# Kernel tuning notes

Measured on AMD Instinct MI355X. Metric: run time of the kernel, lower is better.

## Reference

```python
import jax, jax.numpy as jnp
import numpy as np

CHEBY = 3  # max_degree / number of Chebyshev polynomial orders
IN_F, OUT_F = 64, 64
B, N = 32, 2048


def setup_inputs() -> dict:
    key = jax.random.key(0)
    k1, k2, k3, k4, k5 = jax.random.split(key, 5)
    stdv = 1.0 / np.sqrt(OUT_F)
    stdv2 = 1.0  # 1/sqrt(K.size(1)) = 1/sqrt(1)
    x = jax.random.normal(k1, (B, N, IN_F), dtype=jnp.float32)
    adj = jax.random.uniform(k2, (B, N, N), dtype=jnp.float32)
    weight = jax.random.uniform(k3, (IN_F, OUT_F), minval=-stdv, maxval=stdv, dtype=jnp.float32)
    K = jax.random.uniform(k4, (CHEBY, 1), minval=-stdv2, maxval=stdv2, dtype=jnp.float32)
    bias = jax.random.uniform(k5, (OUT_F,), minval=-stdv, maxval=stdv, dtype=jnp.float32)
    return {"x": x, "adj": adj, "weight": weight, "K": K, "bias": bias}


def chebyshev_stack(x, adj, max_degree):
    # T_0 = x, T_1 = A x, T_k = 2 A T_{k-1} - T_{k-2}; stack along new last axis
    Ts = [x]
    if max_degree > 1:
        Ts.append(jnp.einsum('bnm,bmf->bnf', adj, x))
    for _ in range(2, max_degree):
        Ts.append(2.0 * jnp.einsum('bnm,bmf->bnf', adj, Ts[-1]) - Ts[-2])
    return jnp.stack(Ts, axis=-1)  # [B, N, F, K]


def reference(x, adj, weight, K, bias):
    support = chebyshev_stack(x, adj, CHEBY)            # [B, N, F, K]
    combined = jnp.einsum('bnfk,ko->bnf', support, K)   # K-weighted sum -> [B, N, F]
    out = jnp.einsum('bnf,fo->bno', combined, weight) + bias
    return out
```

## Files before the change

### kernel.cpp

```cpp
#include <hip/hip_runtime.h>
#include <stdint.h>

#define NN 2048
#define FF 64
#define NB 32

typedef __attribute__((ext_vector_type(8))) short bf16x8;
typedef __attribute__((ext_vector_type(4))) float f32x4;

__device__ __forceinline__ uint16_t f2bf(float f) {
  uint32_t u = __builtin_bit_cast(uint32_t, f);
  return (uint16_t)((u + 0x7FFFu + ((u >> 16) & 1u)) >> 16);
}
__device__ __forceinline__ float bf2f(uint16_t h) {
  uint32_t u = ((uint32_t)h) << 16;
  return __builtin_bit_cast(float, u);
}

__global__ void k_prep(const float* __restrict__ W, uint16_t* __restrict__ Wt) {
  int t = threadIdx.x;
  for (int i = 0; i < 16; ++i) {
    int idx = t * 16 + i;
    int k = idx >> 6, f = idx & 63;
    Wt[f * 64 + k] = f2bf(W[idx]);
  }
}

__global__ __launch_bounds__(256) void k_xw(const float* __restrict__ x,
                                            const uint16_t* __restrict__ Wt,
                                            uint16_t* __restrict__ xw) {
  __shared__ short As[64 * 72];
  int bid = blockIdx.x;
  int b = bid >> 5;
  int n0 = (bid & 31) * 64;
  int t = threadIdx.x;
  const float* xb = x + ((size_t)b * NN + n0) * FF;
  for (int i = 0; i < 4; ++i) {
    int idx = t + i * 256;
    int r = idx >> 4, c = (idx & 15) * 4;
    float4 v = *(const float4*)(xb + r * FF + c);
    uint32_t p0 = f2bf(v.x) | ((uint32_t)f2bf(v.y) << 16);
    uint32_t p1 = f2bf(v.z) | ((uint32_t)f2bf(v.w) << 16);
    uint2 pv = {p0, p1};
    *(uint2*)&As[r * 72 + c] = pv;
  }
  __syncthreads();
  int lane = t & 63, wave = t >> 6;
  int l16 = lane & 15, quad = lane >> 4;
  f32x4 acc[4] = {};
  for (int ks = 0; ks < 2; ++ks) {
    bf16x8 a = *(const bf16x8*)&As[(wave * 16 + l16) * 72 + ks * 32 + quad * 8];
    for (int fi = 0; fi < 4; ++fi) {
      bf16x8 bq = *(const bf16x8*)(Wt + (fi * 16 + l16) * 64 + ks * 32 + quad * 8);
      acc[fi] = __builtin_amdgcn_mfma_f32_16x16x32_bf16(a, bq, acc[fi], 0, 0, 0);
    }
  }
  for (int fi = 0; fi < 4; ++fi)
    for (int r = 0; r < 4; ++r) {
      int n = n0 + wave * 16 + quad * 4 + r;
      int f = fi * 16 + l16;
      xw[((size_t)b * NN + n) * FF + f] = f2bf(acc[fi][r]);
    }
}

__global__ __launch_bounds__(256) void k_tr(const uint16_t* __restrict__ src,
                                            uint16_t* __restrict__ dst) {
  __shared__ uint16_t T[64 * 72];
  int bid = blockIdx.x;
  int b = bid >> 5;
  int n0 = (bid & 31) * 64;
  int t = threadIdx.x;
  for (int j = 0; j < 2; ++j) {
    int n = (t >> 3) + j * 32;
    int f8 = (t & 7) * 8;
    uint4 v = *(const uint4*)(src + ((size_t)b * NN + n0 + n) * FF + f8);
    *(uint4*)&T[n * 72 + f8] = v;
  }
  __syncthreads();
  for (int j = 0; j < 2; ++j) {
    int f = (t >> 3) + j * 32;
    int n8 = (t & 7) * 8;
    uint4 v;
    uint16_t* tp = (uint16_t*)&v;
    for (int i = 0; i < 8; ++i) tp[i] = T[(n8 + i) * 72 + f];
    *(uint4*)(dst + ((size_t)b * FF + f) * NN + n0 + n8) = v;
  }
}

template <int EPI>
__global__ __launch_bounds__(256) void k_gemm(const float* __restrict__ adj,
                                              const uint16_t* __restrict__ Bt,
                                              uint16_t* __restrict__ Yb,
                                              const uint16_t* __restrict__ xw,
                                              const uint16_t* __restrict__ y1,
                                              const float* __restrict__ Kc,
                                              const float* __restrict__ bias,
                                              float* __restrict__ out) {
  __shared__ short As[128 * 72];
  __shared__ short Bs[64 * 72];
  int bid = blockIdx.x;
  int b = bid & 31;
  int row0 = (bid >> 5) * 128;
  int t = threadIdx.x;
  const float* Ab = adj + (size_t)b * NN * NN + (size_t)row0 * NN;
  const uint16_t* Btb = Bt + (size_t)b * FF * NN;

  int ar = t >> 4, ac4 = (t & 15) * 4;
  int bfb = t >> 3, bc8 = (t & 7) * 8;

  float4 areg[8];
  uint4 breg[2];
  for (int i = 0; i < 8; ++i)
    areg[i] = *(const float4*)(Ab + (size_t)(ar + i * 16) * NN + ac4);
  for (int j = 0; j < 2; ++j)
    breg[j] = *(const uint4*)(Btb + (size_t)(bfb + j * 32) * NN + bc8);

  f32x4 acc[2][4] = {};
  int lane = t & 63, wave = t >> 6;
  int l16 = lane & 15, quad = lane >> 4;

  for (int k0 = 0; k0 < NN; k0 += 64) {
    __syncthreads();
    for (int i = 0; i < 8; ++i) {
      float4 v = areg[i];
      uint32_t p0 = f2bf(v.x) | ((uint32_t)f2bf(v.y) << 16);
      uint32_t p1 = f2bf(v.z) | ((uint32_t)f2bf(v.w) << 16);
      uint2 pv = {p0, p1};
      *(uint2*)&As[(ar + i * 16) * 72 + ac4] = pv;
    }
    for (int j = 0; j < 2; ++j)
      *(uint4*)&Bs[(bfb + j * 32) * 72 + bc8] = breg[j];
    __syncthreads();
    if (k0 + 64 < NN) {
      for (int i = 0; i < 8; ++i)
        areg[i] = *(const float4*)(Ab + (size_t)(ar + i * 16) * NN + (k0 + 64) + ac4);
      for (int j = 0; j < 2; ++j)
        breg[j] = *(const uint4*)(Btb + (size_t)(bfb + j * 32) * NN + (k0 + 64) + bc8);
    }
    for (int ks = 0; ks < 2; ++ks) {
      bf16x8 af[2];
      for (int mi = 0; mi < 2; ++mi)
        af[mi] = *(const bf16x8*)&As[(wave * 32 + mi * 16 + l16) * 72 + ks * 32 + quad * 8];
      for (int fi = 0; fi < 4; ++fi) {
        bf16x8 bq = *(const bf16x8*)&Bs[(fi * 16 + l16) * 72 + ks * 32 + quad * 8];
        acc[0][fi] = __builtin_amdgcn_mfma_f32_16x16x32_bf16(af[0], bq, acc[0][fi], 0, 0, 0);
        acc[1][fi] = __builtin_amdgcn_mfma_f32_16x16x32_bf16(af[1], bq, acc[1][fi], 0, 0, 0);
      }
    }
  }

  if (EPI == 0) {
    for (int mi = 0; mi < 2; ++mi)
      for (int fi = 0; fi < 4; ++fi)
        for (int r = 0; r < 4; ++r) {
          int n = row0 + wave * 32 + mi * 16 + quad * 4 + r;
          int f = fi * 16 + l16;
          Yb[((size_t)b * NN + n) * FF + f] = f2bf(acc[mi][fi][r]);
        }
  } else {
    float ka = Kc[0] - Kc[2], kb = Kc[1], kc = 2.0f * Kc[2];
    for (int mi = 0; mi < 2; ++mi)
      for (int fi = 0; fi < 4; ++fi) {
        int f = fi * 16 + l16;
        float bv = bias[f];
        for (int r = 0; r < 4; ++r) {
          int n = row0 + wave * 32 + mi * 16 + quad * 4 + r;
          size_t idx = ((size_t)b * NN + n) * FF + f;
          out[idx] = ka * bf2f(xw[idx]) + kb * bf2f(y1[idx]) + kc * acc[mi][fi][r] + bv;
        }
      }
  }
}

extern "C" void kernel_launch(void* const* d_in, const int* in_sizes, int n_in,
                              void* d_out, int out_size, void* d_ws, size_t ws_size,
                              hipStream_t stream) {
  const float* x    = (const float*)d_in[0];
  const float* adj  = (const float*)d_in[1];
  const float* W    = (const float*)d_in[2];
  const float* K    = (const float*)d_in[3];
  const float* bias = (const float*)d_in[4];
  float* out = (float*)d_out;

  uint8_t* ws = (uint8_t*)d_ws;
  const size_t SZ = (size_t)NB * NN * FF * sizeof(uint16_t);
  uint16_t* xw_n = (uint16_t*)(ws);
  uint16_t* xwT  = (uint16_t*)(ws + SZ);
  uint16_t* y1_n = (uint16_t*)(ws + 2 * SZ);
  uint16_t* y1T  = (uint16_t*)(ws + 3 * SZ);
  uint16_t* Wt   = (uint16_t*)(ws + 4 * SZ);

  k_prep<<<dim3(1), dim3(256), 0, stream>>>(W, Wt);
  k_xw<<<dim3(1024), dim3(256), 0, stream>>>(x, Wt, xw_n);
  k_tr<<<dim3(1024), dim3(256), 0, stream>>>(xw_n, xwT);
  k_gemm<0><<<dim3(512), dim3(256), 0, stream>>>(adj, xwT, y1_n, nullptr, nullptr,
                                                 nullptr, nullptr, nullptr);
  k_tr<<<dim3(1024), dim3(256), 0, stream>>>(y1_n, y1T);
  k_gemm<1><<<dim3(512), dim3(256), 0, stream>>>(adj, y1T, nullptr, xw_n, y1_n,
                                                 K, bias, out);
}
```

Measured before the change: 936.4 us.

## Retile adjacency GEMM to 16-row blocks and fuse transposes into producers

The GEMM kernels now use 16-row tiles with 4096 blocks, each wave owning 16 output features. The B operand is read straight from global memory rather than staged in LDS, and A is staged in 256-wide K chunks. The separate transpose kernels are removed: the xw kernel and the first GEMM epilogue each write both the row-major and the transposed copy through a small LDS tile. This aims to raise occupancy and cut launches and extra passes over memory for this bandwidth-bound fp32 adj read, at the cost of less B reuse per block and more global reads of the B operand.

```diff
diff --git a/kernel.cpp b/kernel.cpp
--- a/kernel.cpp
+++ b/kernel.cpp
@@ -26,149 +26,125 @@
   }
 }
 
-__global__ __launch_bounds__(256) void k_xw(const float* __restrict__ x,
-                                            const uint16_t* __restrict__ Wt,
-                                            uint16_t* __restrict__ xw) {
-  __shared__ short As[64 * 72];
+__global__ __launch_bounds__(256, 4) void k_xw(const float* __restrict__ x,
+                                               const uint16_t* __restrict__ Wt,
+                                               uint16_t* __restrict__ xw_n,
+                                               uint16_t* __restrict__ xwT) {
+  __shared__ short Xs[16 * 72];
+  __shared__ short T[64 * 20];
   int bid = blockIdx.x;
-  int b = bid >> 5;
-  int n0 = (bid & 31) * 64;
+  int b = bid & 31;
+  int row0 = (bid >> 5) * 16;
   int t = threadIdx.x;
-  const float* xb = x + ((size_t)b * NN + n0) * FF;
-  for (int i = 0; i < 4; ++i) {
-    int idx = t + i * 256;
-    int r = idx >> 4, c = (idx & 15) * 4;
-    float4 v = *(const float4*)(xb + r * FF + c);
-    uint32_t p0 = f2bf(v.x) | ((uint32_t)f2bf(v.y) << 16);
-    uint32_t p1 = f2bf(v.z) | ((uint32_t)f2bf(v.w) << 16);
-    uint2 pv = {p0, p1};
-    *(uint2*)&As[r * 72 + c] = pv;
+  int lane = t & 63, wv = t >> 6, l16 = lane & 15, quad = lane >> 4;
+
+  int sr = t >> 4, sc = (t & 15) * 4;
+  float4 v = *(const float4*)(x + ((size_t)b * NN + row0 + sr) * FF + sc);
+  uint32_t p0 = f2bf(v.x) | ((uint32_t)f2bf(v.y) << 16);
+  uint32_t p1 = f2bf(v.z) | ((uint32_t)f2bf(v.w) << 16);
+  uint2 pv = {p0, p1};
+  *(uint2*)&Xs[sr * 72 + sc] = pv;
+  __syncthreads();
+
+  f32x4 acc = {};
+#pragma unroll
+  for (int s = 0; s < 2; ++s) {
+    bf16x8 a = *(const bf16x8*)&Xs[l16 * 72 + s * 32 + quad * 8];
+    bf16x8 bq = *(const bf16x8*)(Wt + (size_t)(wv * 16 + l16) * 64 + s * 32 + quad * 8);
+    acc = __builtin_amdgcn_mfma_f32_16x16x32_bf16(a, bq, acc, 0, 0, 0);
   }
+  int f = wv * 16 + l16;
+#pragma unroll
+  for (int r = 0; r < 4; ++r)
+    xw_n[((size_t)b * NN + row0 + quad * 4 + r) * FF + f] = f2bf(acc[r]);
+  uint32_t q0 = f2bf(acc[0]) | ((uint32_t)f2bf(acc[1]) << 16);
+  uint32_t q1 = f2bf(acc[2]) | ((uint32_t)f2bf(acc[3]) << 16);
+  uint2 qv = {q0, q1};
+  *(uint2*)&T[f * 20 + quad * 4] = qv;
   __syncthreads();
-  int lane = t & 63, wave = t >> 6;
-  int l16 = lane & 15, quad = lane >> 4;
-  f32x4 acc[4] = {};
-  for (int ks = 0; ks < 2; ++ks) {
-    bf16x8 a = *(const bf16x8*)&As[(wave * 16 + l16) * 72 + ks * 32 + quad * 8];
-    for (int fi = 0; fi < 4; ++fi) {
-      bf16x8 bq = *(const bf16x8*)(Wt + (fi * 16 + l16) * 64 + ks * 32 + quad * 8);
-      acc[fi] = __builtin_amdgcn_mfma_f32_16x16x32_bf16(a, bq, acc[fi], 0, 0, 0);
-    }
-  }
-  for (int fi = 0; fi < 4; ++fi)
-    for (int r = 0; r < 4; ++r) {
-      int n = n0 + wave * 16 + quad * 4 + r;
-      int f = fi * 16 + l16;
-      xw[((size_t)b * NN + n) * FF + f] = f2bf(acc[fi][r]);
-    }
-}
-
-__global__ __launch_bounds__(256) void k_tr(const uint16_t* __restrict__ src,
-                                            uint16_t* __restrict__ dst) {
-  __shared__ uint16_t T[64 * 72];
-  int bid = blockIdx.x;
-  int b = bid >> 5;
-  int n0 = (bid & 31) * 64;
-  int t = threadIdx.x;
-  for (int j = 0; j < 2; ++j) {
-    int n = (t >> 3) + j * 32;
-    int f8 = (t & 7) * 8;
-    uint4 v = *(const uint4*)(src + ((size_t)b * NN + n0 + n) * FF + f8);
-    *(uint4*)&T[n * 72 + f8] = v;
-  }
-  __syncthreads();
-  for (int j = 0; j < 2; ++j) {
-    int f = (t >> 3) + j * 32;
-    int n8 = (t & 7) * 8;
-    uint4 v;
-    uint16_t* tp = (uint16_t*)&v;
-    for (int i = 0; i < 8; ++i) tp[i] = T[(n8 + i) * 72 + f];
-    *(uint4*)(dst + ((size_t)b * FF + f) * NN + n0 + n8) = v;
-  }
+  int f2 = t >> 2, nc = (t & 3) * 4;
+  uint2 w2 = *(const uint2*)&T[f2 * 20 + nc];
+  *(uint2*)(xwT + ((size_t)b * FF + f2) * NN + row0 + nc) = w2;
 }
 
 template <int EPI>
-__global__ __launch_bounds__(256) void k_gemm(const float* __restrict__ adj,
-                                              const uint16_t* __restrict__ Bt,
-                                              uint16_t* __restrict__ Yb,
-                                              const uint16_t* __restrict__ xw,
-                                              const uint16_t* __restrict__ y1,
-                                              const float* __restrict__ Kc,
-                                              const float* __restrict__ bias,
-                                              float* __restrict__ out) {
-  __shared__ short As[128 * 72];
-  __shared__ short Bs[64 * 72];
+__global__ __launch_bounds__(256, 4) void k_gemm(const float* __restrict__ adj,
+                                                 const uint16_t* __restrict__ Bt,
+                                                 uint16_t* __restrict__ Yn,
+                                                 uint16_t* __restrict__ Yt,
+                                                 const uint16_t* __restrict__ xw,
+                                                 const uint16_t* __restrict__ y1,
+                                                 const float* __restrict__ Kc,
+                                                 const float* __restrict__ bias,
+                                                 float* __restrict__ out) {
+  __shared__ short As[16 * 264];
+  __shared__ short T[64 * 20];
   int bid = blockIdx.x;
   int b = bid & 31;
-  int row0 = (bid >> 5) * 128;
+  int row0 = (bid >> 5) * 16;
   int t = threadIdx.x;
+  int lane = t & 63, wv = t >> 6, l16 = lane & 15, quad = lane >> 4;
+
   const float* Ab = adj + (size_t)b * NN * NN + (size_t)row0 * NN;
-  const uint16_t* Btb = Bt + (size_t)b * FF * NN;
+  const uint16_t* Bb = Bt + (size_t)b * FF * NN + (size_t)(wv * 16 + l16) * NN;
 
-  int ar = t >> 4, ac4 = (t & 15) * 4;
-  int bfb = t >> 3, bc8 = (t & 7) * 8;
+  int sr = t >> 4;
+  int sc = (t & 15) * 16;
+  const float* ap = Ab + (size_t)sr * NN + sc;
 
-  float4 areg[8];
-  uint4 breg[2];
-  for (int i = 0; i < 8; ++i)
-    areg[i] = *(const float4*)(Ab + (size_t)(ar + i * 16) * NN + ac4);
-  for (int j = 0; j < 2; ++j)
-    breg[j] = *(const uint4*)(Btb + (size_t)(bfb + j * 32) * NN + bc8);
+  float4 areg[4];
+#pragma unroll
+  for (int i = 0; i < 4; ++i) areg[i] = *(const float4*)(ap + i * 4);
 
-  f32x4 acc[2][4] = {};
-  int lane = t & 63, wave = t >> 6;
-  int l16 = lane & 15, quad = lane >> 4;
-
-  for (int k0 = 0; k0 < NN; k0 += 64) {
+  f32x4 acc = {};
+  for (int kc = 0; kc < 8; ++kc) {
     __syncthreads();
-    for (int i = 0; i < 8; ++i) {
-      float4 v = areg[i];
-      uint32_t p0 = f2bf(v.x) | ((uint32_t)f2bf(v.y) << 16);
-      uint32_t p1 = f2bf(v.z) | ((uint32_t)f2bf(v.w) << 16);
-      uint2 pv = {p0, p1};
-      *(uint2*)&As[(ar + i * 16) * 72 + ac4] = pv;
+    uint32_t p[8];
+#pragma unroll
+    for (int i = 0; i < 4; ++i) {
+      p[2 * i]     = f2bf(areg[i].x) | ((uint32_t)f2bf(areg[i].y) << 16);
+      p[2 * i + 1] = f2bf(areg[i].z) | ((uint32_t)f2bf(areg[i].w) << 16);
     }
-    for (int j = 0; j < 2; ++j)
-      *(uint4*)&Bs[(bfb + j * 32) * 72 + bc8] = breg[j];
+    uint4 w0 = {p[0], p[1], p[2], p[3]};
+    uint4 w1 = {p[4], p[5], p[6], p[7]};
+    ((uint4*)&As[sr * 264 + sc])[0] = w0;
+    ((uint4*)&As[sr * 264 + sc])[1] = w1;
     __syncthreads();
-    if (k0 + 64 < NN) {
-      for (int i = 0; i < 8; ++i)
-        areg[i] = *(const float4*)(Ab + (size_t)(ar + i * 16) * NN + (k0 + 64) + ac4);
-      for (int j = 0; j < 2; ++j)
-        breg[j] = *(const uint4*)(Btb + (size_t)(bfb + j * 32) * NN + (k0 + 64) + bc8);
+    if (kc < 7) {
+      const float* np = ap + (kc + 1) * 256;
+#pragma unroll
+      for (int i = 0; i < 4; ++i) areg[i] = *(const float4*)(np + i * 4);
     }
-    for (int ks = 0; ks < 2; ++ks) {
-      bf16x8 af[2];
-      for (int mi = 0; mi < 2; ++mi)
-        af[mi] = *(const bf16x8*)&As[(wave * 32 + mi * 16 + l16) * 72 + ks * 32 + quad * 8];
-      for (int fi = 0; fi < 4; ++fi) {
-        bf16x8 bq = *(const bf16x8*)&Bs[(fi * 16 + l16) * 72 + ks * 32 + quad * 8];
-        acc[0][fi] = __builtin_amdgcn_mfma_f32_16x16x32_bf16(af[0], bq, acc[0][fi], 0, 0, 0);
-        acc[1][fi] = __builtin_amdgcn_mfma_f32_16x16x32_bf16(af[1], bq, acc[1][fi], 0, 0, 0);
-      }
+    const uint16_t* brow = Bb + kc * 256;
+#pragma unroll
+    for (int s = 0; s < 8; ++s) {
+      bf16x8 a = *(const bf16x8*)&As[l16 * 264 + s * 32 + quad * 8];
+      bf16x8 bq = *(const bf16x8*)(brow + s * 32 + quad * 8);
+      acc = __builtin_amdgcn_mfma_f32_16x16x32_bf16(a, bq, acc, 0, 0, 0);
     }
   }
 
+  int f = wv * 16 + l16;
   if (EPI == 0) {
-    for (int mi = 0; mi < 2; ++mi)
-      for (int fi = 0; fi < 4; ++fi)
-        for (int r = 0; r < 4; ++r) {
-          int n = row0 + wave * 32 + mi * 16 + quad * 4 + r;
-          int f = fi * 16 + l16;
-          Yb[((size_t)b * NN + n) * FF + f] = f2bf(acc[mi][fi][r]);
-        }
+#pragma unroll
+    for (int r = 0; r < 4; ++r)
+      Yn[((size_t)b * NN + row0 + quad * 4 + r) * FF + f] = f2bf(acc[r]);
+    uint32_t q0 = f2bf(acc[0]) | ((uint32_t)f2bf(acc[1]) << 16);
+    uint32_t q1 = f2bf(acc[2]) | ((uint32_t)f2bf(acc[3]) << 16);
+    uint2 qv = {q0, q1};
+    *(uint2*)&T[f * 20 + quad * 4] = qv;
+    __syncthreads();
+    int f2 = t >> 2, nc = (t & 3) * 4;
+    uint2 w2 = *(const uint2*)&T[f2 * 20 + nc];
+    *(uint2*)(Yt + ((size_t)b * FF + f2) * NN + row0 + nc) = w2;
   } else {
-    float ka = Kc[0] - Kc[2], kb = Kc[1], kc = 2.0f * Kc[2];
-    for (int mi = 0; mi < 2; ++mi)
-      for (int fi = 0; fi < 4; ++fi) {
-        int f = fi * 16 + l16;
-        float bv = bias[f];
-        for (int r = 0; r < 4; ++r) {
-          int n = row0 + wave * 32 + mi * 16 + quad * 4 + r;
-          size_t idx = ((size_t)b * NN + n) * FF + f;
-          out[idx] = ka * bf2f(xw[idx]) + kb * bf2f(y1[idx]) + kc * acc[mi][fi][r] + bv;
-        }
-      }
+    float ka = Kc[0] - Kc[2], kb = Kc[1], kc2 = 2.0f * Kc[2];
+    float bv = bias[f];
+#pragma unroll
+    for (int r = 0; r < 4; ++r) {
+      size_t idx = ((size_t)b * NN + row0 + quad * 4 + r) * FF + f;
+      out[idx] = ka * bf2f(xw[idx]) + kb * bf2f(y1[idx]) + kc2 * acc[r] + bv;
+    }
   }
 }
 
@@ -191,11 +167,9 @@
   uint16_t* Wt   = (uint16_t*)(ws + 4 * SZ);
 
   k_prep<<<dim3(1), dim3(256), 0, stream>>>(W, Wt);
-  k_xw<<<dim3(1024), dim3(256), 0, stream>>>(x, Wt, xw_n);
-  k_tr<<<dim3(1024), dim3(256), 0, stream>>>(xw_n, xwT);
-  k_gemm<0><<<dim3(512), dim3(256), 0, stream>>>(adj, xwT, y1_n, nullptr, nullptr,
-                                                 nullptr, nullptr, nullptr);
-  k_tr<<<dim3(1024), dim3(256), 0, stream>>>(y1_n, y1T);
-  k_gemm<1><<<dim3(512), dim3(256), 0, stream>>>(adj, y1T, nullptr, xw_n, y1_n,
-                                                 K, bias, out);
+  k_xw<<<dim3(4096), dim3(256), 0, stream>>>(x, Wt, xw_n, xwT);
+  k_gemm<0><<<dim3(4096), dim3(256), 0, stream>>>(adj, xwT, y1_n, y1T,
+                                                  nullptr, nullptr, nullptr, nullptr, nullptr);
+  k_gemm<1><<<dim3(4096), dim3(256), 0, stream>>>(adj, y1T, nullptr, nullptr,
+                                                  xw_n, y1_n, K, bias, out);
 }
```

After: 969.2 us. 3.5% more time.
